# Optimization experiments

Measured on AMD Instinct MI355X. Metric: run time of the kernel, lower is better.

Reference implementation:

```python
import jax, jax.numpy as jnp
import numpy as np

D_MODEL = 1024
D_STATE = 16
D_CONV = 4
D_INNER = 2 * D_MODEL
DT_RANK = 64
BATCH = 2
SEQ = 1024
EPS = 1e-6


def setup_inputs() -> dict:
    key = jax.random.key(0)
    ks = jax.random.split(key, 8)
    s = 0.02
    return {
        "x": jax.random.normal(ks[0], (BATCH, SEQ, D_MODEL), jnp.float32),
        "norm_w": jnp.ones((D_MODEL,), jnp.float32),
        "in_proj_w": jax.random.normal(ks[1], (2 * D_INNER, D_MODEL), jnp.float32) * s,
        "conv_w": jax.random.normal(ks[2], (D_INNER, 1, D_CONV), jnp.float32) * s,
        "conv_b": jnp.zeros((D_INNER,), jnp.float32),
        "x_proj_w": jax.random.normal(ks[3], (DT_RANK + 2 * D_STATE, D_INNER), jnp.float32) * s,
        "dt_proj_w": jax.random.normal(ks[4], (D_INNER, DT_RANK), jnp.float32) * s,
        "dt_proj_b": jnp.zeros((D_INNER,), jnp.float32),
        "A_log": jnp.tile(jnp.log(jnp.arange(1, D_STATE + 1, dtype=jnp.float32)), (D_INNER, 1)),
        "D_diag": jnp.ones((D_INNER,), jnp.float32),
        "out_proj_w": jax.random.normal(ks[5], (D_MODEL, D_INNER), jnp.float32) * s,
    }


def reference(x, norm_w, in_proj_w, conv_w, conv_b, x_proj_w, dt_proj_w, dt_proj_b, A_log, D_diag, out_proj_w):
    residual = x
    # RMSNorm
    ms = jnp.mean(x * x, axis=-1, keepdims=True)
    xn = x * jax.lax.rsqrt(ms + EPS) * norm_w
    # in_proj -> split into x branch and gate z
    xz = xn @ in_proj_w.T  # [B, L, 2*d_inner]
    xc, z = jnp.split(xz, 2, axis=-1)
    # depthwise causal conv1d with padding d_conv-1, truncated to L
    xc = xc.transpose(0, 2, 1)  # [B, d_inner, L]
    conv = jax.lax.conv_general_dilated(
        xc, conv_w, window_strides=(1,), padding=[(D_CONV - 1, D_CONV - 1)],
        feature_group_count=D_INNER, dimension_numbers=("NCH", "OIH", "NCH"))
    conv = conv[:, :, :SEQ] + conv_b[None, :, None]
    u = jax.nn.silu(conv.transpose(0, 2, 1))  # [B, L, d_inner]
    # input-dependent dt, B, C
    proj = u @ x_proj_w.T  # [B, L, dt_rank + 2*d_state]
    dt_raw = proj[..., :DT_RANK]
    b_raw = proj[..., DT_RANK:DT_RANK + D_STATE]
    c_raw = proj[..., DT_RANK + D_STATE:]
    dt = jax.nn.softplus(dt_raw @ dt_proj_w.T + dt_proj_b)  # [B, L, d_inner]
    A = -jnp.exp(A_log)  # [d_inner, d_state]

    def step(state, inp):
        dt_t, u_t, b_t, c_t = inp  # [B,d], [B,d], [B,n], [B,n]
        dA = jnp.exp(dt_t[:, :, None] * A)  # [B, d, n]
        state = dA * state + dt_t[:, :, None] * b_t[:, None, :] * u_t[:, :, None]
        y_t = jnp.einsum("bdn,bn->bd", state, c_t) + D_diag * u_t
        return state, y_t

    xs = (dt.transpose(1, 0, 2), u.transpose(1, 0, 2),
          b_raw.transpose(1, 0, 2), c_raw.transpose(1, 0, 2))
    state0 = jnp.zeros((x.shape[0], D_INNER, D_STATE), x.dtype)
    _, ys = jax.lax.scan(step, state0, xs)  # ys: [L, B, d_inner]
    y = ys.transpose(1, 0, 2)
    y = y * jax.nn.silu(z)
    y = y @ out_proj_w.T
    return residual + y
```

## Files before the change

kernel.cpp:

```cpp
#include <hip/hip_runtime.h>
#include <hip/hip_bf16.h>
#include <math.h>

#define D_MODEL 1024
#define D_STATE 16
#define D_CONV 4
#define D_INNER 2048
#define DT_RANK 64
#define BATCH 2
#define SEQ 1024
#define NTOK (BATCH * SEQ)
#define XPROJ_N (DT_RANK + 2 * D_STATE)
#define EPS 1e-6f

#define NCHUNK 32
#define CHLEN (SEQ / NCHUNK)

#define XK_SPLIT 16
#define OK_SPLIT 2

typedef __attribute__((ext_vector_type(8))) short bf16x8;
typedef __attribute__((ext_vector_type(4))) float f32x4;
typedef __hip_bfloat16 bf16;

__device__ inline void gload_lds16(const void* g, void* l) {
  __builtin_amdgcn_global_load_lds(
      (const __attribute__((address_space(1))) void*)g,
      (__attribute__((address_space(3))) void*)l, 16, 0, 0);
}

__device__ inline unsigned short f2bfu(float f) {
  bf16 h = __float2bfloat16(f);
  return *(unsigned short*)&h;
}

__device__ inline float bfu2f(short s) {
  bf16 h;
  *(short*)&h = s;
  return __bfloat162float(h);
}

#define WS0 (4096 * 1024)
#define WS1 (96 * 2048)
#define WS2 (2048 * 64)
#define WS3 (1024 * 2048)
#define NWCONV ((WS0 + WS1 + WS2 + WS3) / 1024)
__global__ __launch_bounds__(256) void prologue_kernel(
    const float* __restrict__ x, const float* __restrict__ nw,
    bf16* __restrict__ xn,
    const float* __restrict__ w0, bf16* __restrict__ o0,
    const float* __restrict__ w1, bf16* __restrict__ o1,
    const float* __restrict__ w2, bf16* __restrict__ o2,
    const float* __restrict__ w3, bf16* __restrict__ o3) {
  int tid = threadIdx.x;
  if (blockIdx.x < NTOK) {
    int token = blockIdx.x;
    const float* xr = x + (size_t)token * D_MODEL;
    float v[4];
    float s = 0.f;
#pragma unroll
    for (int i = 0; i < 4; ++i) {
      v[i] = xr[tid + i * 256];
      s += v[i] * v[i];
    }
#pragma unroll
    for (int off = 32; off > 0; off >>= 1) s += __shfl_down(s, off, 64);
    __shared__ float warp_s[4];
    if ((tid & 63) == 0) warp_s[tid >> 6] = s;
    __syncthreads();
    float total = warp_s[0] + warp_s[1] + warp_s[2] + warp_s[3];
    float scale = rsqrtf(total / (float)D_MODEL + EPS);
    bf16* xo = xn + (size_t)token * D_MODEL;
#pragma unroll
    for (int i = 0; i < 4; ++i)
      xo[tid + i * 256] = __float2bfloat16(v[i] * scale * nw[tid + i * 256]);
  } else {
    int base = ((blockIdx.x - NTOK) * 256 + tid) * 4;
    const float* in;
    bf16* out;
    int off;
    if (base < WS0) {
      in = w0; out = o0; off = base;
    } else if (base < WS0 + WS1) {
      in = w1; out = o1; off = base - WS0;
    } else if (base < WS0 + WS1 + WS2) {
      in = w2; out = o2; off = base - WS0 - WS1;
    } else {
      in = w3; out = o3; off = base - WS0 - WS1 - WS2;
    }
    float4 v = *(const float4*)(in + off);
    ushort4 o;
    o.x = f2bfu(v.x); o.y = f2bfu(v.y); o.z = f2bfu(v.z); o.w = f2bfu(v.w);
    *(ushort4*)(out + off) = o;
  }
}

template <int EPI, int BM, int BN, int BK>
__global__ __launch_bounds__(256) void gemm_bf16(
    const bf16* __restrict__ A, int lda, const bf16* __restrict__ B, int ldb,
    bf16* __restrict__ C, int ldc, int M, int N, int K,
    const float* __restrict__ bias, const float* __restrict__ resid) {
  constexpr int AI = BM / 32;
  constexpr int NJ = BN / 32;
  constexpr int KV = BK / 8;
  constexpr int AL = BM * BK / 2048;
  constexpr int BL = BN * BK / 2048;
  __shared__ bf16 As[2][BM * BK];
  __shared__ bf16 Bs[2][BN * BK];
  const int tid = threadIdx.x;
  const int lane = tid & 63;
  const int wave = tid >> 6;
  const int wm = wave >> 1;
  const int wn = wave & 1;
  const int bm = blockIdx.y;
  const int bn = blockIdx.x;

  f32x4 acc[AI][NJ] = {};

  const int kchunk = K / (int)gridDim.z;
  const int kb = blockIdx.z * kchunk;
  const int kend = kb + kchunk;

  const int lrow = lane & 15;
  const int lk = (lane >> 4) * 8;

  auto stage = [&](int buf, int k0) {
#pragma unroll
    for (int r = 0; r < AL; ++r) {
      int idx = r * 256 + tid;
      int row = idx / KV;
      int kc = (idx % KV) * 8;
      int kcs = kc ^ ((row & (KV - 1)) * 8);
      gload_lds16(A + (size_t)(bm * BM + row) * lda + k0 + kcs,
                  &As[buf][idx * 8]);
    }
#pragma unroll
    for (int r = 0; r < BL; ++r) {
      int idx = r * 256 + tid;
      int row = idx / KV;
      int kc = (idx % KV) * 8;
      int kcs = kc ^ ((row & (KV - 1)) * 8);
      gload_lds16(B + (size_t)(bn * BN + row) * ldb + k0 + kcs,
                  &Bs[buf][idx * 8]);
    }
  };

  stage(0, kb);
  asm volatile("s_waitcnt vmcnt(0)\ns_barrier" ::: "memory");

  int cur = 0;
  for (int k0 = kb; k0 < kend; k0 += BK) {
    if (k0 + BK < kend) stage(cur ^ 1, k0 + BK);

#pragma unroll
    for (int ks = 0; ks < BK / 32; ++ks) {
      bf16x8 a[AI], b[NJ];
#pragma unroll
      for (int i = 0; i < AI; ++i) {
        int row = wm * (BM / 2) + i * 16 + lrow;
        a[i] = *(const bf16x8*)(
            &As[cur][row * BK + ((ks * 32 + lk) ^ ((row & (KV - 1)) * 8))]);
      }
#pragma unroll
      for (int j = 0; j < NJ; ++j) {
        int row = wn * (BN / 2) + j * 16 + lrow;
        b[j] = *(const bf16x8*)(
            &Bs[cur][row * BK + ((ks * 32 + lk) ^ ((row & (KV - 1)) * 8))]);
      }
#pragma unroll
      for (int i = 0; i < AI; ++i)
#pragma unroll
        for (int j = 0; j < NJ; ++j)
          acc[i][j] = __builtin_amdgcn_mfma_f32_16x16x32_bf16(a[i], b[j],
                                                              acc[i][j], 0, 0, 0);
    }

    asm volatile("s_waitcnt vmcnt(0)\ns_barrier" ::: "memory");
    cur ^= 1;
  }

#pragma unroll
  for (int j = 0; j < NJ; ++j) {
    int col = bn * BN + wn * (BN / 2) + j * 16 + lrow;
    if (col < N) {
      float bv = (EPI == 1) ? bias[col] : 0.f;
#pragma unroll
      for (int i = 0; i < AI; ++i) {
#pragma unroll
        for (int reg = 0; reg < 4; ++reg) {
          int row = bm * BM + wm * (BM / 2) + i * 16 + (lane >> 4) * 4 + reg;
          float v = acc[i][j][reg];
          if (EPI == 1) {
            v += bv;
            v = (v > 20.f) ? v : log1pf(__expf(v));
          }
          if (EPI == 2) {
            ((float*)C)[(size_t)row * ldc + col] =
                v + resid[(size_t)row * ldc + col];
          } else if (EPI == 3) {
            C[((size_t)blockIdx.z * M + row) * ldc + col] = __float2bfloat16(v);
          } else {
            C[(size_t)row * ldc + col] = __float2bfloat16(v);
          }
        }
      }
    }
  }
}

__global__ __launch_bounds__(256) void reduce_proj_kernel(
    const bf16* __restrict__ part, bf16* __restrict__ projbf) {
  int i = blockIdx.x * 256 + threadIdx.x;
  float s = 0.f;
#pragma unroll
  for (int z = 0; z < XK_SPLIT; ++z)
    s += __bfloat162float(part[(size_t)z * NTOK * XPROJ_N + i]);
  projbf[i] = __float2bfloat16(s);
}

__global__ __launch_bounds__(256) void reduce_out_kernel(
    const bf16* __restrict__ part, const float* __restrict__ resid,
    float* __restrict__ out) {
  int i = (blockIdx.x * 256 + threadIdx.x) * 8;
  bf16x8 p0 = *(const bf16x8*)(part + i);
  bf16x8 p1 = *(const bf16x8*)(part + (size_t)NTOK * D_MODEL + i);
  float4 r0 = *(const float4*)(resid + i);
  float4 r1 = *(const float4*)(resid + i + 4);
  float4 o0, o1;
  o0.x = bfu2f(p0[0]) + bfu2f(p1[0]) + r0.x;
  o0.y = bfu2f(p0[1]) + bfu2f(p1[1]) + r0.y;
  o0.z = bfu2f(p0[2]) + bfu2f(p1[2]) + r0.z;
  o0.w = bfu2f(p0[3]) + bfu2f(p1[3]) + r0.w;
  o1.x = bfu2f(p0[4]) + bfu2f(p1[4]) + r1.x;
  o1.y = bfu2f(p0[5]) + bfu2f(p1[5]) + r1.y;
  o1.z = bfu2f(p0[6]) + bfu2f(p1[6]) + r1.z;
  o1.w = bfu2f(p0[7]) + bfu2f(p1[7]) + r1.w;
  *(float4*)(out + i) = o0;
  *(float4*)(out + i + 4) = o1;
}

__global__ __launch_bounds__(256) void conv_silu_kernel(
    const bf16* __restrict__ xz, const float* __restrict__ cw,
    const float* __restrict__ cb, bf16* __restrict__ u) {
  int id = blockIdx.x * 256 + threadIdx.x;
  int c8 = id & 255;
  int token = id >> 8;
  int d0 = c8 * 8;
  int t = token & (SEQ - 1);

  float acc[8];
  {
    float4 b0 = *(const float4*)(cb + d0);
    float4 b1 = *(const float4*)(cb + d0 + 4);
    acc[0] = b0.x; acc[1] = b0.y; acc[2] = b0.z; acc[3] = b0.w;
    acc[4] = b1.x; acc[5] = b1.y; acc[6] = b1.z; acc[7] = b1.w;
  }
  float4 wv[8];
#pragma unroll
  for (int k = 0; k < 8; ++k) wv[k] = *(const float4*)(cw + (d0 + k) * 4);

#pragma unroll
  for (int j = 0; j < D_CONV; ++j) {
    int tt = t - (D_CONV - 1) + j;
    if (tt >= 0) {
      bf16x8 v = *(const bf16x8*)(xz + (size_t)(token - (D_CONV - 1) + j) * 4096 + d0);
#pragma unroll
      for (int k = 0; k < 8; ++k)
        acc[k] = fmaf(((const float*)&wv[k])[j], bfu2f(v[k]), acc[k]);
    }
  }

  bf16x8 o;
#pragma unroll
  for (int k = 0; k < 8; ++k) {
    float s = acc[k] / (1.f + __expf(-acc[k]));
    o[k] = (short)f2bfu(s);
  }
  *(bf16x8*)(u + (size_t)token * D_INNER + d0) = o;
}

__global__ __launch_bounds__(256) void scan_pass1(
    const bf16* __restrict__ projbf, const bf16* __restrict__ dtb,
    const bf16* __restrict__ u,
    bf16* __restrict__ s_end, bf16* __restrict__ decay) {
  int tid = threadIdx.x;
  int d = blockIdx.x * 256 + tid;
  int c = blockIdx.y;
  int b = blockIdx.z;
  size_t tok0 = (size_t)b * SEQ + (size_t)c * CHLEN;

  __shared__ float Bs[CHLEN][D_STATE];
  for (int i = tid; i < CHLEN * D_STATE; i += 256) {
    int t = i >> 4, n = i & 15;
    Bs[t][n] = __bfloat162float(projbf[(tok0 + t) * XPROJ_N + DT_RANK + n]);
  }
  __syncthreads();

  float st[16];
#pragma unroll
  for (int n = 0; n < 16; ++n) st[n] = 0.f;
  float dtsum = 0.f;

  for (int t = 0; t < CHLEN; ++t) {
    float dtv = __bfloat162float(dtb[(tok0 + t) * D_INNER + d]);
    float uv = __bfloat162float(u[(tok0 + t) * D_INNER + d]);
    float dtu = dtv * uv;
    dtsum += dtv;
    float e = __expf(-dtv);
    float dAn = 1.f;
#pragma unroll
    for (int n = 0; n < 16; ++n) {
      dAn *= e;
      st[n] = fmaf(dAn, st[n], dtu * Bs[t][n]);
    }
  }

  size_t base = (((size_t)b * NCHUNK + c) * D_INNER + d) * D_STATE;
  float E = __expf(-dtsum);
  float dE = 1.f;
#pragma unroll
  for (int n = 0; n < 16; ++n) {
    dE *= E;
    s_end[base + n] = __float2bfloat16(st[n]);
    decay[base + n] = __float2bfloat16(dE);
  }
}

__global__ __launch_bounds__(256) void scan_pass2(
    const bf16* __restrict__ s_end, const bf16* __restrict__ decay,
    bf16* __restrict__ s0) {
  int gid = blockIdx.x * 256 + threadIdx.x;
  int b = gid >> 15;
  int dn = gid & (D_INNER * D_STATE - 1);
  float s = 0.f;
  for (int c = 0; c < NCHUNK; ++c) {
    size_t idx = ((size_t)(b * NCHUNK + c) * D_INNER * D_STATE) + dn;
    s0[idx] = __float2bfloat16(s);
    s = fmaf(__bfloat162float(decay[idx]), s, __bfloat162float(s_end[idx]));
  }
}

__global__ __launch_bounds__(256) void scan_pass3(
    const bf16* __restrict__ projbf, const bf16* __restrict__ dtb,
    const bf16* __restrict__ u, const bf16* __restrict__ xz,
    const float* __restrict__ D_diag,
    const bf16* __restrict__ s0, bf16* __restrict__ y) {
  int tid = threadIdx.x;
  int d = blockIdx.x * 256 + tid;
  int c = blockIdx.y;
  int b = blockIdx.z;
  size_t tok0 = (size_t)b * SEQ + (size_t)c * CHLEN;

  __shared__ float BC[CHLEN][2 * D_STATE];
  for (int i = tid; i < CHLEN * 2 * D_STATE; i += 256) {
    int t = i >> 5, col = i & 31;
    BC[t][col] = __bfloat162float(projbf[(tok0 + t) * XPROJ_N + DT_RANK + col]);
  }
  __syncthreads();

  float st[16];
  size_t base = (((size_t)b * NCHUNK + c) * D_INNER + d) * D_STATE;
#pragma unroll
  for (int n = 0; n < 16; ++n) st[n] = __bfloat162float(s0[base + n]);
  float Dd = D_diag[d];

  for (int t = 0; t < CHLEN; ++t) {
    size_t tok = tok0 + t;
    float dtv = __bfloat162float(dtb[tok * D_INNER + d]);
    float uv = __bfloat162float(u[tok * D_INNER + d]);
    float zv = __bfloat162float(xz[tok * (2 * D_INNER) + D_INNER + d]);
    float dtu = dtv * uv;
    float yv = Dd * uv;
    float e = __expf(-dtv);
    float dAn = 1.f;
#pragma unroll
    for (int n = 0; n < 16; ++n) {
      dAn *= e;
      st[n] = fmaf(dAn, st[n], dtu * BC[t][n]);
      yv = fmaf(st[n], BC[t][D_STATE + n], yv);
    }
    y[tok * D_INNER + d] = __float2bfloat16(yv * (zv / (1.f + __expf(-zv))));
  }
}

extern "C" void kernel_launch(void* const* d_in, const int* in_sizes, int n_in,
                              void* d_out, int out_size, void* d_ws,
                              size_t ws_size, hipStream_t stream) {
  const float* x         = (const float*)d_in[0];
  const float* norm_w    = (const float*)d_in[1];
  const float* in_proj_w = (const float*)d_in[2];
  const float* conv_w    = (const float*)d_in[3];
  const float* conv_b    = (const float*)d_in[4];
  const float* x_proj_w  = (const float*)d_in[5];
  const float* dt_proj_w = (const float*)d_in[6];
  const float* dt_proj_b = (const float*)d_in[7];
  const float* D_diag    = (const float*)d_in[9];
  const float* out_proj_w= (const float*)d_in[10];
  float* out = (float*)d_out;

  char* p = (char*)d_ws;
  bf16* xz    = (bf16*)p;  p += (size_t)NTOK * 4096 * 2;
  bf16* dt    = (bf16*)p;  p += (size_t)NTOK * D_INNER * 2;
  bf16* projbf= (bf16*)p;  p += (size_t)NTOK * XPROJ_N * 2;
  bf16* u_bf  = (bf16*)p;  p += (size_t)NTOK * D_INNER * 2;
  bf16* ybuf  = (bf16*)p;  p += (size_t)NTOK * D_INNER * 2;
  bf16* in_w  = (bf16*)p;  p += (size_t)4096 * 1024 * 2;
  bf16* xw    = (bf16*)p;  p += (size_t)128 * 2048 * 2;
  bf16* dtw   = (bf16*)p;  p += (size_t)2048 * 64 * 2;
  bf16* ow    = (bf16*)p;  p += (size_t)1024 * 2048 * 2;
  char* un = p;
  const size_t AGGB = (size_t)BATCH * NCHUNK * D_INNER * D_STATE * 2;
  bf16* ppart = (bf16*)un;
  bf16* xn_bf = (bf16*)(un + (size_t)XK_SPLIT * NTOK * XPROJ_N * 2);
  bf16* s_end = (bf16*)un;
  bf16* decay = (bf16*)(un + AGGB);
  bf16* s0    = (bf16*)(un + 2 * AGGB);
  bf16* opart = (bf16*)(un + 3 * AGGB);

  prologue_kernel<<<NTOK + NWCONV, 256, 0, stream>>>(
      x, norm_w, xn_bf, in_proj_w, in_w, x_proj_w, xw, dt_proj_w, dtw,
      out_proj_w, ow);

  {
    dim3 grid(4096 / 128, NTOK / 128, 1);
    gemm_bf16<0, 128, 128, 64><<<grid, 256, 0, stream>>>(
        xn_bf, D_MODEL, in_w, D_MODEL, xz, 2 * D_INNER, NTOK, 2 * D_INNER,
        D_MODEL, nullptr, nullptr);
  }

  conv_silu_kernel<<<NTOK, 256, 0, stream>>>(xz, conv_w, conv_b, u_bf);

  {
    dim3 grid(1, NTOK / 64, XK_SPLIT);
    gemm_bf16<3, 64, 128, 64><<<grid, 256, 0, stream>>>(
        u_bf, D_INNER, xw, D_INNER, ppart, XPROJ_N, NTOK, XPROJ_N, D_INNER,
        nullptr, nullptr);
    reduce_proj_kernel<<<NTOK * XPROJ_N / 256, 256, 0, stream>>>(ppart,
                                                                 projbf);
  }

  {
    dim3 grid(D_INNER / 64, NTOK / 128, 1);
    gemm_bf16<1, 128, 64, 64><<<grid, 256, 0, stream>>>(
        projbf, XPROJ_N, dtw, DT_RANK, dt, D_INNER, NTOK, D_INNER, DT_RANK,
        dt_proj_b, nullptr);
  }

  {
    dim3 grid(D_INNER / 256, NCHUNK, BATCH);
    scan_pass1<<<grid, 256, 0, stream>>>(projbf, dt, u_bf, s_end, decay);
    scan_pass2<<<BATCH * D_INNER * D_STATE / 256, 256, 0, stream>>>(s_end,
                                                                    decay, s0);
    scan_pass3<<<grid, 256, 0, stream>>>(projbf, dt, u_bf, xz, D_diag, s0,
                                         ybuf);
  }

  {
    dim3 grid(D_MODEL / 64, NTOK / 128, OK_SPLIT);
    gemm_bf16<3, 128, 64, 64><<<grid, 256, 0, stream>>>(
        ybuf, D_INNER, ow, D_INNER, opart, D_MODEL, NTOK, D_MODEL, D_INNER,
        nullptr, nullptr);
    reduce_out_kernel<<<NTOK * D_MODEL / 2048, 256, 0, stream>>>(opart, x, out);
  }
}
```

Before: 139.8 us.

## Add multi-stage LDS pipelining to bf16 GEMM and shrink in_proj N-tile

Generalizes the GEMM from double-buffering to a DEPTH-slot ring of shared-memory buffers. Partial vmcnt waits let up to DEPTH-1 tiles of global->LDS loads stay in flight, and the barrier moves to the top of each iteration so only one sync per tile remains. All GEMMs use DEPTH=3, which raises LDS use per block and may lower occupancy. The in_proj GEMM also switches from 128x128 to 128x64 tiles, doubling the grid to improve CU fill at the cost of more A-tile reloads.

```diff
diff --git a/kernel.cpp b/kernel.cpp
--- a/kernel.cpp
+++ b/kernel.cpp
@@ -95,7 +95,7 @@
   }
 }
 
-template <int EPI, int BM, int BN, int BK>
+template <int EPI, int BM, int BN, int BK, int DEPTH>
 __global__ __launch_bounds__(256) void gemm_bf16(
     const bf16* __restrict__ A, int lda, const bf16* __restrict__ B, int ldb,
     bf16* __restrict__ C, int ldc, int M, int N, int K,
@@ -105,8 +105,9 @@
   constexpr int KV = BK / 8;
   constexpr int AL = BM * BK / 2048;
   constexpr int BL = BN * BK / 2048;
-  __shared__ bf16 As[2][BM * BK];
-  __shared__ bf16 Bs[2][BN * BK];
+  constexpr int LOADS = AL + BL;
+  __shared__ bf16 As[DEPTH][BM * BK];
+  __shared__ bf16 Bs[DEPTH][BN * BK];
   const int tid = threadIdx.x;
   const int lane = tid & 63;
   const int wave = tid >> 6;
@@ -119,7 +120,7 @@
 
   const int kchunk = K / (int)gridDim.z;
   const int kb = blockIdx.z * kchunk;
-  const int kend = kb + kchunk;
+  const int ntiles = kchunk / BK;
 
   const int lrow = lane & 15;
   const int lk = (lane >> 4) * 8;
@@ -145,12 +146,28 @@
     }
   };
 
-  stage(0, kb);
-  asm volatile("s_waitcnt vmcnt(0)\ns_barrier" ::: "memory");
+#pragma unroll
+  for (int t = 0; t < DEPTH - 1; ++t)
+    if (t < ntiles) stage(t, kb + t * BK);
 
   int cur = 0;
-  for (int k0 = kb; k0 < kend; k0 += BK) {
-    if (k0 + BK < kend) stage(cur ^ 1, k0 + BK);
+  for (int t = 0; t < ntiles; ++t) {
+    int ahead = ntiles - 1 - t;
+    if (ahead >= DEPTH - 2) {
+      asm volatile("s_waitcnt vmcnt(%0)" ::"i"((DEPTH - 2) * LOADS)
+                   : "memory");
+    } else if (DEPTH > 3 && ahead == 1) {
+      asm volatile("s_waitcnt vmcnt(%0)" ::"i"(LOADS) : "memory");
+    } else {
+      asm volatile("s_waitcnt vmcnt(0)" ::: "memory");
+    }
+    asm volatile("s_barrier" ::: "memory");
+
+    if (t + DEPTH - 1 < ntiles) {
+      int sslot = cur + DEPTH - 1;
+      if (sslot >= DEPTH) sslot -= DEPTH;
+      stage(sslot, kb + (t + DEPTH - 1) * BK);
+    }
 
 #pragma unroll
     for (int ks = 0; ks < BK / 32; ++ks) {
@@ -175,8 +192,7 @@
                                                               acc[i][j], 0, 0, 0);
     }
 
-    asm volatile("s_waitcnt vmcnt(0)\ns_barrier" ::: "memory");
-    cur ^= 1;
+    cur = (cur + 1 == DEPTH) ? 0 : cur + 1;
   }
 
 #pragma unroll
@@ -422,8 +438,8 @@
       out_proj_w, ow);
 
   {
-    dim3 grid(4096 / 128, NTOK / 128, 1);
-    gemm_bf16<0, 128, 128, 64><<<grid, 256, 0, stream>>>(
+    dim3 grid(4096 / 64, NTOK / 128, 1);
+    gemm_bf16<0, 128, 64, 64, 3><<<grid, 256, 0, stream>>>(
         xn_bf, D_MODEL, in_w, D_MODEL, xz, 2 * D_INNER, NTOK, 2 * D_INNER,
         D_MODEL, nullptr, nullptr);
   }
@@ -432,7 +448,7 @@
 
   {
     dim3 grid(1, NTOK / 64, XK_SPLIT);
-    gemm_bf16<3, 64, 128, 64><<<grid, 256, 0, stream>>>(
+    gemm_bf16<3, 64, 128, 64, 3><<<grid, 256, 0, stream>>>(
         u_bf, D_INNER, xw, D_INNER, ppart, XPROJ_N, NTOK, XPROJ_N, D_INNER,
         nullptr, nullptr);
     reduce_proj_kernel<<<NTOK * XPROJ_N / 256, 256, 0, stream>>>(ppart,
@@ -441,7 +457,7 @@
 
   {
     dim3 grid(D_INNER / 64, NTOK / 128, 1);
-    gemm_bf16<1, 128, 64, 64><<<grid, 256, 0, stream>>>(
+    gemm_bf16<1, 128, 64, 64, 3><<<grid, 256, 0, stream>>>(
         projbf, XPROJ_N, dtw, DT_RANK, dt, D_INNER, NTOK, D_INNER, DT_RANK,
         dt_proj_b, nullptr);
   }
@@ -457,7 +473,7 @@
 
   {
     dim3 grid(D_MODEL / 64, NTOK / 128, OK_SPLIT);
-    gemm_bf16<3, 128, 64, 64><<<grid, 256, 0, stream>>>(
+    gemm_bf16<3, 128, 64, 64, 3><<<grid, 256, 0, stream>>>(
         ybuf, D_INNER, ow, D_INNER, opart, D_MODEL, NTOK, D_MODEL, D_INNER,
         nullptr, nullptr);
     reduce_out_kernel<<<NTOK * D_MODEL / 2048, 256, 0, stream>>>(opart, x, out);
```

New measurement: 146.7 us. 1.05x slower.
